# Performance work log

Hardware: AMD Instinct MI355X
Metric: run time of the kernel (lower is better)

The kernel has to match this reference:

```python
import jax, jax.numpy as jnp
import numpy as np

S_IN = 10.0   # sharpness_inside
S_OUT = 10.0  # sharpness_outside
NEG_FILL = -100.0  # value written outside the ellipsoid mask


def _quat_to_rot(q):
    # q: (B, M, 4) -> (B, M, 3, 3)
    q = q / jnp.linalg.norm(q, axis=-1, keepdims=True)
    w, x, y, z = q[..., 0], q[..., 1], q[..., 2], q[..., 3]
    R = jnp.stack([
        1 - 2 * (y * y + z * z), 2 * (x * y - w * z), 2 * (x * z + w * y),
        2 * (x * y + w * z), 1 - 2 * (x * x + z * z), 2 * (y * z - w * x),
        2 * (x * z - w * y), 2 * (y * z + w * x), 1 - 2 * (x * x + y * y),
    ], axis=-1)
    return R.reshape(q.shape[:-1] + (3, 3))


def setup_inputs() -> dict:
    key = jax.random.key(0)
    ks = jax.random.split(key, 12)
    B, N, P, M, C, H = 2, 256, 32, 16, 128, 256

    def lin(k, fan_in, shape):
        return (jax.random.normal(k, shape, jnp.float32) / np.sqrt(fan_in)).astype(jnp.float32)

    return {
        'ray_points': jax.random.normal(ks[0], (B, N, P, 3), jnp.float32),
        'translations': 0.5 * jax.random.normal(ks[1], (B, M, 3), jnp.float32),
        'rotations': jax.random.normal(ks[2], (B, M, 4), jnp.float32),
        'scale': 0.2 + 0.8 * jax.random.uniform(ks[3], (B, M, 3), jnp.float32),
        'part_shape_features': jax.random.normal(ks[4], (B, M, C), jnp.float32),
        'Wp': lin(ks[5], 3, (3, H)),   'bp': jnp.zeros((H,), jnp.float32),
        'Wc': lin(ks[6], C, (C, H)),   'bc': jnp.zeros((H,), jnp.float32),
        'W1': lin(ks[7], H, (H, H)),   'b1': jnp.zeros((H,), jnp.float32),
        'W2': lin(ks[8], H, (H, H)),   'b2': jnp.zeros((H,), jnp.float32),
        'Wout': lin(ks[9], H, (H, 1)), 'bout': jnp.zeros((1,), jnp.float32),
    }


def reference(ray_points, translations, rotations, scale, part_shape_features,
              Wp, bp, Wc, bc, W1, b1, W2, b2, Wout, bout):
    B, N, P, _ = ray_points.shape
    M = translations.shape[1]
    pts = ray_points.reshape(B, N * P, 3)

    # transform_to_primitives_centric_system: R @ (x - t)
    Xc = pts[:, :, None, :] - translations[:, None, :, :]          # (B, Np, M, 3)
    R = _quat_to_rot(rotations)                                    # (B, M, 3, 3)
    Xt = jnp.einsum('bmij,bnmj->bnmi', R, Xc)                      # (B, Np, M, 3)

    # inside_outside_function_ellipsoid: F = sum((x/a)^2)
    F_ell = jnp.sum((Xt / scale[:, None, :, :]) ** 2, axis=-1)     # (B, Np, M)
    mask = F_ell <= 1.0

    # MiniOccupancyNet: fc_p + per-block conditioning + resnet block + fc_out
    net = jnp.einsum('bnmd,dh->bnmh', Xt, Wp) + bp                 # (B, Np, M, H)
    cond = jnp.einsum('bmc,ch->bmh', part_shape_features, Wc) + bc # (B, M, H)
    net = net + cond[:, None, :, :]
    dx = jax.nn.relu(net) @ W1 + b1
    dx = jax.nn.relu(dx) @ W2 + b2
    net = net + dx
    occ = (jax.nn.relu(net) @ Wout + bout)[..., 0]                 # (B, Np, M)

    # masked gather-compute-scatter == dense compute + fill -100 outside mask
    F = jnp.where(mask, occ, NEG_FILL)

    # apply_sigmoid_to_inside_outside_function: piecewise sharpness
    sharp = jnp.where(F > 0, S_IN, S_OUT)
    implicit = jax.nn.sigmoid(sharp * F)                           # (B, Np, M)
    return implicit.reshape(B, N, P, M)
```

## Files before the change

### kernel.cpp

```cpp
#include <hip/hip_runtime.h>
#include <hip/hip_fp16.h>
#include <math.h>

#define B_   2
#define N_   256
#define P_   32
#define M_   16
#define C_   128
#define H_   256
#define NP_  (N_ * P_)
#define ROWS_ (B_ * NP_ * M_)
#define HALF_ (ROWS_ / 2)
#define TM_  64
#define LDA_ (H_ + 8)
#define MROWS_ 1024

typedef _Float16 half8 __attribute__((ext_vector_type(8)));
typedef float f32x4 __attribute__((ext_vector_type(4)));

__global__ __launch_bounds__(256)
void prep_mask_k(const float* __restrict__ W1, const float* __restrict__ W2,
                 _Float16* __restrict__ Wt1, _Float16* __restrict__ Wt2,
                 const float* __restrict__ psf, const float* __restrict__ Wc,
                 const float* __restrict__ bc, const float* __restrict__ Wp,
                 const float* __restrict__ bp, _Float16* __restrict__ B0t,
                 const float* __restrict__ pts, const float* __restrict__ trans,
                 const float* __restrict__ rots, const float* __restrict__ scal,
                 int* __restrict__ cnt, int* __restrict__ wl) {
    __shared__ float t[64][65];
    const int tid = threadIdx.x;

    if (blockIdx.x < 32) {
        const int id = blockIdx.x;
        const float* W = (id & 1) ? W2 : W1;
        _Float16* Wt = (id & 1) ? Wt2 : Wt1;
        const int tile = id >> 1, I = tile >> 2, J = tile & 3;
        const int r = tid >> 6, c = tid & 63;
        #pragma unroll
        for (int p = 0; p < 16; ++p)
            t[p * 4 + r][c] = W[(I * 64 + p * 4 + r) * H_ + J * 64 + c];
        __syncthreads();
        #pragma unroll
        for (int p = 0; p < 16; ++p)
            Wt[(J * 64 + p * 4 + r) * H_ + I * 64 + c] = (_Float16)t[c][p * 4 + r];
        return;
    }
    if (blockIdx.x < 64) {
        const int bm = blockIdx.x - 32;
        const int b = bm >> 4, m = bm & 15;
        const int h = tid;
        const float* p = psf + bm * C_;
        float acc = bc[h];
        for (int c = 0; c < C_; ++c) acc += p[c] * Wc[c * H_ + h];
        _Float16* dst = B0t + (b * H_ + h) * 32;
        dst[3 + m] = (_Float16)(acc + bp[h]);
        if (m == 0) {
            dst[0] = (_Float16)Wp[h];
            dst[1] = (_Float16)Wp[H_ + h];
            dst[2] = (_Float16)Wp[2 * H_ + h];
            #pragma unroll
            for (int k = 19; k < 32; ++k) dst[k] = (_Float16)0.0f;
        }
        return;
    }

    float (*sR)[9] = (float (*)[9])&t[0][0];
    float (*sT)[3] = (float (*)[3])&t[4][0];
    float (*sS)[3] = (float (*)[3])&t[8][0];
    __shared__ int sBuf[MROWS_];
    __shared__ int sCnt;
    __shared__ int sBase;

    const int base = (blockIdx.x - 64) * MROWS_;
    const int b    = base >> 17;

    if (tid == 0) sCnt = 0;
    if (tid < M_) {
        const int m = tid;
        const float* q = rots + (b * M_ + m) * 4;
        float w = q[0], x = q[1], y = q[2], z = q[3];
        float nrm = sqrtf(w * w + x * x + y * y + z * z);
        w /= nrm; x /= nrm; y /= nrm; z /= nrm;
        sR[m][0] = 1.0f - 2.0f * (y * y + z * z);
        sR[m][1] = 2.0f * (x * y - w * z);
        sR[m][2] = 2.0f * (x * z + w * y);
        sR[m][3] = 2.0f * (x * y + w * z);
        sR[m][4] = 1.0f - 2.0f * (x * x + z * z);
        sR[m][5] = 2.0f * (y * z - w * x);
        sR[m][6] = 2.0f * (x * z - w * y);
        sR[m][7] = 2.0f * (y * z + w * x);
        sR[m][8] = 1.0f - 2.0f * (x * x + y * y);
        const float* tp = trans + (b * M_ + m) * 3;
        sT[m][0] = tp[0]; sT[m][1] = tp[1]; sT[m][2] = tp[2];
        const float* sp = scal + (b * M_ + m) * 3;
        sS[m][0] = sp[0]; sS[m][1] = sp[1]; sS[m][2] = sp[2];
    }
    __syncthreads();

    const int m = tid & (M_ - 1);
    #pragma unroll
    for (int r = 0; r < 4; ++r) {
        const int row = base + r * 256 + tid;
        const int gp  = row >> 4;
        float fe;
        {
            #pragma clang fp contract(off)
            const float* p = pts + gp * 3;
            float x0 = p[0] - sT[m][0];
            float x1 = p[1] - sT[m][1];
            float x2 = p[2] - sT[m][2];
            float t0 = sR[m][0] * x0 + sR[m][1] * x1 + sR[m][2] * x2;
            float t1 = sR[m][3] * x0 + sR[m][4] * x1 + sR[m][5] * x2;
            float t2 = sR[m][6] * x0 + sR[m][7] * x1 + sR[m][8] * x2;
            float v0 = t0 / sS[m][0];
            float v1 = t1 / sS[m][1];
            float v2 = t2 / sS[m][2];
            fe = v0 * v0 + v1 * v1 + v2 * v2;
        }
        if (fe <= 1.0f) {
            const int pos = atomicAdd(&sCnt, 1);
            sBuf[pos] = row;
        }
    }
    __syncthreads();
    if (tid == 0) sBase = sCnt ? atomicAdd(&cnt[b], sCnt) : 0;
    __syncthreads();
    const int tot = sCnt, gb = b * HALF_ + sBase;
    for (int i = tid; i < tot; i += 256) wl[gb + i] = sBuf[i];
}

__global__ __launch_bounds__(256, 2)
void occ_k(const float* __restrict__ pts,  const float* __restrict__ trans,
           const float* __restrict__ rots, const float* __restrict__ scal,
           const float* __restrict__ b1v,  const float* __restrict__ b2v,
           const float* __restrict__ Wout, const float* __restrict__ bout,
           const _Float16* __restrict__ Wt1, const _Float16* __restrict__ Wt2,
           const _Float16* __restrict__ B0t, const int* __restrict__ cnt,
           const int* __restrict__ wl, float* __restrict__ out) {
    const int half = blockIdx.x >> 8;
    const int j0   = blockIdx.x & 255;
    const int count = cnt[half];
    if (j0 * TM_ >= count) return;

    __shared__ __align__(16) _Float16 sA0[TM_][32];
    __shared__ __align__(16) _Float16 sAbuf[TM_][LDA_];
    __shared__ float sR[M_][9];
    __shared__ float sT[M_][3];
    __shared__ float sS[M_][3];
    __shared__ float sPart[TM_][4];
    __shared__ int   sIdx[TM_];

    const int tid = threadIdx.x;
    const int b   = half;

    if (tid < M_) {
        const int m = tid;
        const float* q = rots + (b * M_ + m) * 4;
        float w = q[0], x = q[1], y = q[2], z = q[3];
        float nrm = sqrtf(w * w + x * x + y * y + z * z);
        w /= nrm; x /= nrm; y /= nrm; z /= nrm;
        sR[m][0] = 1.0f - 2.0f * (y * y + z * z);
        sR[m][1] = 2.0f * (x * y - w * z);
        sR[m][2] = 2.0f * (x * z + w * y);
        sR[m][3] = 2.0f * (x * y + w * z);
        sR[m][4] = 1.0f - 2.0f * (x * x + z * z);
        sR[m][5] = 2.0f * (y * z - w * x);
        sR[m][6] = 2.0f * (x * z - w * y);
        sR[m][7] = 2.0f * (y * z + w * x);
        sR[m][8] = 1.0f - 2.0f * (x * x + y * y);
        const float* tp = trans + (b * M_ + m) * 3;
        sT[m][0] = tp[0]; sT[m][1] = tp[1]; sT[m][2] = tp[2];
        const float* sp = scal + (b * M_ + m) * 3;
        sS[m][0] = sp[0]; sS[m][1] = sp[1]; sS[m][2] = sp[2];
    }

    const int w    = tid >> 6;
    const int lane = tid & 63;
    const int quad = lane >> 4;
    const int ln   = lane & 15;
    const f32x4 zero = {0.0f, 0.0f, 0.0f, 0.0f};

    for (int j = j0; j * TM_ < count; j += 256) {
        __syncthreads();
        if (tid < TM_) {
            const int k = j * TM_ + tid;
            sIdx[tid] = (k < count) ? wl[half * HALF_ + k] : -1;
        }
        __syncthreads();

        {
            const int r  = tid >> 2;
            const int kg = tid & 3;
            const int idx  = sIdx[r];
            const int safe = idx < 0 ? 0 : idx;
            const int m  = safe & (M_ - 1);
            const int gp = safe >> 4;
            half8 av;
            #pragma unroll
            for (int jj = 0; jj < 8; ++jj) av[jj] = (_Float16)0.0f;
            if (kg == 0) {
                float t0, t1, t2;
                {
                    #pragma clang fp contract(off)
                    const float* p = pts + gp * 3;
                    float x0 = p[0] - sT[m][0];
                    float x1 = p[1] - sT[m][1];
                    float x2 = p[2] - sT[m][2];
                    t0 = sR[m][0] * x0 + sR[m][1] * x1 + sR[m][2] * x2;
                    t1 = sR[m][3] * x0 + sR[m][4] * x1 + sR[m][5] * x2;
                    t2 = sR[m][6] * x0 + sR[m][7] * x1 + sR[m][8] * x2;
                }
                av[0] = (_Float16)t0; av[1] = (_Float16)t1; av[2] = (_Float16)t2;
                #pragma unroll
                for (int jj = 3; jj < 8; ++jj) av[jj] = (m == jj - 3) ? (_Float16)1.0f : (_Float16)0.0f;
            } else if (kg == 1) {
                #pragma unroll
                for (int jj = 0; jj < 8; ++jj) av[jj] = (m == 5 + jj) ? (_Float16)1.0f : (_Float16)0.0f;
            } else if (kg == 2) {
                #pragma unroll
                for (int jj = 0; jj < 3; ++jj) av[jj] = (m == 13 + jj) ? (_Float16)1.0f : (_Float16)0.0f;
            }
            *(half8*)&sA0[r][kg * 8] = av;
        }
        __syncthreads();

        f32x4 acc0[4][4];
        {
            half8 a0[4], b0[4];
            #pragma unroll
            for (int rt = 0; rt < 4; ++rt)
                a0[rt] = *(const half8*)&sA0[rt * 16 + ln][quad * 8];
            const _Float16* B0w = B0t + (b * H_ + w * 64) * 32 + quad * 8;
            #pragma unroll
            for (int tc = 0; tc < 4; ++tc)
                b0[tc] = *(const half8*)(B0w + (tc * 16 + ln) * 32);
            #pragma unroll
            for (int rt = 0; rt < 4; ++rt)
                #pragma unroll
                for (int tc = 0; tc < 4; ++tc)
                    acc0[rt][tc] = __builtin_amdgcn_mfma_f32_16x16x32_f16(a0[rt], b0[tc], zero, 0, 0, 0);

            #pragma unroll
            for (int tc = 0; tc < 4; ++tc) {
                const int col = w * 64 + tc * 16 + ln;
                #pragma unroll
                for (int rt = 0; rt < 4; ++rt)
                    #pragma unroll
                    for (int rg = 0; rg < 4; ++rg) {
                        float v = acc0[rt][tc][rg];
                        v = v > 0.0f ? v : 0.0f;
                        sAbuf[rt * 16 + quad * 4 + rg][col] = (_Float16)v;
                    }
            }
        }
        __syncthreads();

        f32x4 acc1[4][4];
        #pragma unroll
        for (int tc = 0; tc < 4; ++tc) {
            const float bb = b1v[w * 64 + tc * 16 + ln];
            const f32x4 bv = {bb, bb, bb, bb};
            #pragma unroll
            for (int rt = 0; rt < 4; ++rt) acc1[rt][tc] = bv;
        }
        {
            const _Float16* Wb1 = Wt1 + (w * 64) * H_;
            #pragma unroll
            for (int kc = 0; kc < 8; ++kc) {
                const int k0 = kc * 32 + quad * 8;
                half8 a[4], bf[4];
                #pragma unroll
                for (int rt = 0; rt < 4; ++rt)
                    a[rt] = *(const half8*)&sAbuf[rt * 16 + ln][k0];
                #pragma unroll
                for (int tc = 0; tc < 4; ++tc)
                    bf[tc] = *(const half8*)(Wb1 + (tc * 16 + ln) * H_ + k0);
                #pragma unroll
                for (int rt = 0; rt < 4; ++rt)
                    #pragma unroll
                    for (int tc = 0; tc < 4; ++tc)
                        acc1[rt][tc] = __builtin_amdgcn_mfma_f32_16x16x32_f16(a[rt], bf[tc], acc1[rt][tc], 0, 0, 0);
            }
        }
        __syncthreads();

        #pragma unroll
        for (int tc = 0; tc < 4; ++tc) {
            const int col = w * 64 + tc * 16 + ln;
            #pragma unroll
            for (int rt = 0; rt < 4; ++rt)
                #pragma unroll
                for (int rg = 0; rg < 4; ++rg) {
                    float v = acc1[rt][tc][rg];
                    v = v > 0.0f ? v : 0.0f;
                    sAbuf[rt * 16 + quad * 4 + rg][col] = (_Float16)v;
                }
        }
        __syncthreads();

        #pragma unroll
        for (int tc = 0; tc < 4; ++tc) {
            const float bb = b2v[w * 64 + tc * 16 + ln];
            const f32x4 bv = {bb, bb, bb, bb};
            #pragma unroll
            for (int rt = 0; rt < 4; ++rt) acc0[rt][tc] += bv;
        }
        {
            const _Float16* Wb2 = Wt2 + (w * 64) * H_;
            #pragma unroll
            for (int kc = 0; kc < 8; ++kc) {
                const int k0 = kc * 32 + quad * 8;
                half8 a[4], bf[4];
                #pragma unroll
                for (int rt = 0; rt < 4; ++rt)
                    a[rt] = *(const half8*)&sAbuf[rt * 16 + ln][k0];
                #pragma unroll
                for (int tc = 0; tc < 4; ++tc)
                    bf[tc] = *(const half8*)(Wb2 + (tc * 16 + ln) * H_ + k0);
                #pragma unroll
                for (int rt = 0; rt < 4; ++rt)
                    #pragma unroll
                    for (int tc = 0; tc < 4; ++tc)
                        acc0[rt][tc] = __builtin_amdgcn_mfma_f32_16x16x32_f16(a[rt], bf[tc], acc0[rt][tc], 0, 0, 0);
            }
        }

        float rowsum[4][4];
        #pragma unroll
        for (int rt = 0; rt < 4; ++rt)
            #pragma unroll
            for (int rg = 0; rg < 4; ++rg) rowsum[rt][rg] = 0.0f;

        #pragma unroll
        for (int tc = 0; tc < 4; ++tc) {
            const float wo = Wout[w * 64 + tc * 16 + ln];
            #pragma unroll
            for (int rt = 0; rt < 4; ++rt)
                #pragma unroll
                for (int rg = 0; rg < 4; ++rg) {
                    float net = acc0[rt][tc][rg];
                    net = net > 0.0f ? net : 0.0f;
                    rowsum[rt][rg] += net * wo;
                }
        }

        #pragma unroll
        for (int rt = 0; rt < 4; ++rt)
            #pragma unroll
            for (int rg = 0; rg < 4; ++rg) {
                float v = rowsum[rt][rg];
                v += __shfl_xor(v, 1, 16);
                v += __shfl_xor(v, 2, 16);
                v += __shfl_xor(v, 4, 16);
                v += __shfl_xor(v, 8, 16);
                if (ln == 0) sPart[rt * 16 + quad * 4 + rg][w] = v;
            }
        __syncthreads();

        if (tid < TM_) {
            const int idx = sIdx[tid];
            if (idx >= 0) {
                float occ = sPart[tid][0] + sPart[tid][1] + sPart[tid][2] + sPart[tid][3] + bout[0];
                out[idx] = 1.0f / (1.0f + __expf(-10.0f * occ));
            }
        }
    }
}

extern "C" void kernel_launch(void* const* d_in, const int* in_sizes, int n_in,
                              void* d_out, int out_size, void* d_ws, size_t ws_size,
                              hipStream_t stream) {
    const float* pts   = (const float*)d_in[0];
    const float* trans = (const float*)d_in[1];
    const float* rots  = (const float*)d_in[2];
    const float* scal  = (const float*)d_in[3];
    const float* psf   = (const float*)d_in[4];
    const float* Wp    = (const float*)d_in[5];
    const float* bp    = (const float*)d_in[6];
    const float* Wc    = (const float*)d_in[7];
    const float* bc    = (const float*)d_in[8];
    const float* W1    = (const float*)d_in[9];
    const float* b1    = (const float*)d_in[10];
    const float* W2    = (const float*)d_in[11];
    const float* b2    = (const float*)d_in[12];
    const float* Wout  = (const float*)d_in[13];
    const float* bout  = (const float*)d_in[14];
    float* out = (float*)d_out;

    char* ws = (char*)d_ws;
    _Float16* Wt1 = (_Float16*)ws;
    _Float16* Wt2 = (_Float16*)(ws + 131072);
    _Float16* B0t = (_Float16*)(ws + 262144);
    int*      cnt = (int*)(ws + 294912);
    int*      wl  = (int*)(ws + 295168);

    hipMemsetAsync(cnt, 0, 2 * sizeof(int), stream);
    hipMemsetAsync(out, 0, (size_t)out_size * sizeof(float), stream);
    hipLaunchKernelGGL(prep_mask_k, dim3(64 + ROWS_ / MROWS_), dim3(256), 0, stream,
                       W1, W2, Wt1, Wt2, psf, Wc, bc, Wp, bp, B0t,
                       pts, trans, rots, scal, cnt, wl);
    hipLaunchKernelGGL(occ_k, dim3(512), dim3(256), 0, stream,
                       pts, trans, rots, scal, b1, b2, Wout, bout,
                       Wt1, Wt2, B0t, cnt, wl, out);
}
```

Measured before the change: 119.8 us.

## Use per-block worklists instead of global atomic compaction and drop memsets

The mask kernel now writes each block's inside rows into a fixed per-block slice of the worklist and records a per-block count, instead of using a global atomic counter per batch. The compute kernel gets one block per mask block and walks that block's own list. The mask kernel also writes zeros for outside rows, so both hipMemsetAsync calls are removed. In exchange, load balance now depends on how many inside rows each 1024-row chunk has, and blocks with few hits leave tiles partly empty.

```diff
diff --git a/kernel.cpp b/kernel.cpp
--- a/kernel.cpp
+++ b/kernel.cpp
@@ -14,6 +14,7 @@
 #define TM_  64
 #define LDA_ (H_ + 8)
 #define MROWS_ 1024
+#define MBLK_ (ROWS_ / MROWS_)
 
 typedef _Float16 half8 __attribute__((ext_vector_type(8)));
 typedef float f32x4 __attribute__((ext_vector_type(4)));
@@ -26,7 +27,8 @@
                  const float* __restrict__ bp, _Float16* __restrict__ B0t,
                  const float* __restrict__ pts, const float* __restrict__ trans,
                  const float* __restrict__ rots, const float* __restrict__ scal,
-                 int* __restrict__ cnt, int* __restrict__ wl) {
+                 int* __restrict__ cntArr, int* __restrict__ wl,
+                 float* __restrict__ out) {
     __shared__ float t[64][65];
     const int tid = threadIdx.x;
 
@@ -69,9 +71,9 @@
     float (*sS)[3] = (float (*)[3])&t[8][0];
     __shared__ int sBuf[MROWS_];
     __shared__ int sCnt;
-    __shared__ int sBase;
-
-    const int base = (blockIdx.x - 64) * MROWS_;
+
+    const int blk  = blockIdx.x - 64;
+    const int base = blk * MROWS_;
     const int b    = base >> 17;
 
     if (tid == 0) sCnt = 0;
@@ -120,13 +122,14 @@
         if (fe <= 1.0f) {
             const int pos = atomicAdd(&sCnt, 1);
             sBuf[pos] = row;
+        } else {
+            out[row] = 0.0f;
         }
     }
     __syncthreads();
-    if (tid == 0) sBase = sCnt ? atomicAdd(&cnt[b], sCnt) : 0;
-    __syncthreads();
-    const int tot = sCnt, gb = b * HALF_ + sBase;
-    for (int i = tid; i < tot; i += 256) wl[gb + i] = sBuf[i];
+    const int tot = sCnt;
+    if (tid == 0) cntArr[blk] = tot;
+    for (int i = tid; i < tot; i += 256) wl[blk * MROWS_ + i] = sBuf[i];
 }
 
 __global__ __launch_bounds__(256, 2)
@@ -135,12 +138,12 @@
            const float* __restrict__ b1v,  const float* __restrict__ b2v,
            const float* __restrict__ Wout, const float* __restrict__ bout,
            const _Float16* __restrict__ Wt1, const _Float16* __restrict__ Wt2,
-           const _Float16* __restrict__ B0t, const int* __restrict__ cnt,
+           const _Float16* __restrict__ B0t, const int* __restrict__ cntArr,
            const int* __restrict__ wl, float* __restrict__ out) {
-    const int half = blockIdx.x >> 8;
-    const int j0   = blockIdx.x & 255;
-    const int count = cnt[half];
-    if (j0 * TM_ >= count) return;
+    const int blk   = blockIdx.x;
+    const int count = cntArr[blk];
+    if (count == 0) return;
+    const int b     = blk >> 7;
 
     __shared__ __align__(16) _Float16 sA0[TM_][32];
     __shared__ __align__(16) _Float16 sAbuf[TM_][LDA_];
@@ -151,7 +154,6 @@
     __shared__ int   sIdx[TM_];
 
     const int tid = threadIdx.x;
-    const int b   = half;
 
     if (tid < M_) {
         const int m = tid;
@@ -180,11 +182,11 @@
     const int ln   = lane & 15;
     const f32x4 zero = {0.0f, 0.0f, 0.0f, 0.0f};
 
-    for (int j = j0; j * TM_ < count; j += 256) {
+    for (int off = 0; off < count; off += TM_) {
         __syncthreads();
         if (tid < TM_) {
-            const int k = j * TM_ + tid;
-            sIdx[tid] = (k < count) ? wl[half * HALF_ + k] : -1;
+            const int k = off + tid;
+            sIdx[tid] = (k < count) ? wl[blk * MROWS_ + k] : -1;
         }
         __syncthreads();
 
@@ -388,18 +390,16 @@
     float* out = (float*)d_out;
 
     char* ws = (char*)d_ws;
-    _Float16* Wt1 = (_Float16*)ws;
-    _Float16* Wt2 = (_Float16*)(ws + 131072);
-    _Float16* B0t = (_Float16*)(ws + 262144);
-    int*      cnt = (int*)(ws + 294912);
-    int*      wl  = (int*)(ws + 295168);
-
-    hipMemsetAsync(cnt, 0, 2 * sizeof(int), stream);
-    hipMemsetAsync(out, 0, (size_t)out_size * sizeof(float), stream);
-    hipLaunchKernelGGL(prep_mask_k, dim3(64 + ROWS_ / MROWS_), dim3(256), 0, stream,
+    _Float16* Wt1    = (_Float16*)ws;
+    _Float16* Wt2    = (_Float16*)(ws + 131072);
+    _Float16* B0t    = (_Float16*)(ws + 262144);
+    int*      cntArr = (int*)(ws + 294912);
+    int*      wl     = (int*)(ws + 295936);
+
+    hipLaunchKernelGGL(prep_mask_k, dim3(64 + MBLK_), dim3(256), 0, stream,
                        W1, W2, Wt1, Wt2, psf, Wc, bc, Wp, bp, B0t,
-                       pts, trans, rots, scal, cnt, wl);
-    hipLaunchKernelGGL(occ_k, dim3(512), dim3(256), 0, stream,
+                       pts, trans, rots, scal, cntArr, wl, out);
+    hipLaunchKernelGGL(occ_k, dim3(MBLK_), dim3(256), 0, stream,
                        pts, trans, rots, scal, b1, b2, Wout, bout,
-                       Wt1, Wt2, B0t, cnt, wl, out);
+                       Wt1, Wt2, B0t, cntArr, wl, out);
 }
```

Measured after the change: 121.0 us. Within noise of the previous version (+1.1%).
